# Kernel tuning notes

Measured on AMD Instinct MI355X. Metric: run time of the kernel, lower is better.

The kernel has to match this reference:

```python
import jax, jax.numpy as jnp
import numpy as np

H = 64
IN_DIM = 32
N = 50000
E = 100000
B = 500


def setup_inputs() -> dict:
    key = jax.random.key(0)
    ks = jax.random.split(key, 16)
    def rn(k, shape, s=0.05):
        return jax.random.normal(k, shape, dtype=jnp.float32) * s
    inp = dict(
        nfeat=rn(ks[0], (N, IN_DIM), 1.0),
        efeat=rn(ks[1], (E, 5), 1.0),
        lin0_w=rn(ks[2], (IN_DIM, H)), lin0_b=jnp.zeros((H,), jnp.float32),
        ew1=rn(ks[3], (5, 128)), eb1=jnp.zeros((128,), jnp.float32),
        ew2=rn(ks[4], (128, H * H)), eb2=jnp.zeros((H * H,), jnp.float32),
        conv_b=jnp.zeros((H,), jnp.float32),
        gru_wih=rn(ks[5], (3 * H, H)), gru_whh=rn(ks[6], (3 * H, H)),
        gru_bih=jnp.zeros((3 * H,), jnp.float32), gru_bhh=jnp.zeros((3 * H,), jnp.float32),
        lstm_wih=rn(ks[7], (4 * H, 2 * H)), lstm_whh=rn(ks[8], (4 * H, H)),
        lstm_bih=jnp.zeros((4 * H,), jnp.float32), lstm_bhh=jnp.zeros((4 * H,), jnp.float32),
        fc1_w=rn(ks[9], (2 * H, H)), fc1_b=jnp.zeros((H,), jnp.float32),
        fc2_w=rn(ks[10], (H, 1)), fc2_b=jnp.zeros((1,), jnp.float32),
        src=jax.random.randint(ks[11], (E,), 0, N),
        dst=jax.random.randint(ks[12], (E,), 0, N),
        graph_id=jnp.arange(N) // (N // B),  # B graphs of equal size, sorted
        num_graphs=B,
    )
    return inp


def reference(nfeat, efeat, lin0_w, lin0_b, ew1, eb1, ew2, eb2, conv_b,
              gru_wih, gru_whh, gru_bih, gru_bhh,
              lstm_wih, lstm_whh, lstm_bih, lstm_bhh,
              fc1_w, fc1_b, fc2_w, fc2_b,
              src, dst, graph_id, num_graphs):
    n_nodes = nfeat.shape[0]
    # lin0 + relu
    h = jax.nn.relu(nfeat @ lin0_w + lin0_b)  # [N, H]
    # edge-conditioned weight matrices (same for all 3 iterations)
    We = (jax.nn.relu(efeat @ ew1 + eb1) @ ew2 + eb2).reshape(-1, H, H)  # [E, H, H]
    deg = jnp.maximum(
        jax.ops.segment_sum(jnp.ones(src.shape[0], jnp.float32), dst, num_segments=n_nodes), 1.0)
    for _ in range(3):
        # NNConv: gather src feats, per-edge matmul, scatter-mean at dst
        msg = jnp.einsum('eh,eho->eo', h[src], We)  # [E, H]
        agg = jax.ops.segment_sum(msg, dst, num_segments=n_nodes) / deg[:, None]
        m = jax.nn.relu(agg + conv_b)
        # GRU step (PyTorch gate order r,z,n)
        gi = m @ gru_wih.T + gru_bih
        gh = h @ gru_whh.T + gru_bhh
        r = jax.nn.sigmoid(gi[:, :H] + gh[:, :H])
        z = jax.nn.sigmoid(gi[:, H:2 * H] + gh[:, H:2 * H])
        n = jnp.tanh(gi[:, 2 * H:] + r * gh[:, 2 * H:])
        h = (1.0 - z) * n + z * h
    feat = h  # [N, H]
    # Set2Set pooling: 3 iters, 1-layer LSTM with input 2H
    q_star = jnp.zeros((num_graphs, 2 * H), jnp.float32)
    hh = jnp.zeros((num_graphs, H), jnp.float32)
    cc = jnp.zeros((num_graphs, H), jnp.float32)
    for _ in range(3):
        gates = q_star @ lstm_wih.T + lstm_bih + hh @ lstm_whh.T + lstm_bhh
        i = jax.nn.sigmoid(gates[:, :H])
        f = jax.nn.sigmoid(gates[:, H:2 * H])
        g = jnp.tanh(gates[:, 2 * H:3 * H])
        o = jax.nn.sigmoid(gates[:, 3 * H:])
        cc = f * cc + i * g
        hh = o * jnp.tanh(cc)
        q = hh  # [B, H]
        e = jnp.sum(feat * q[graph_id], axis=-1)  # [N]
        emax = jax.ops.segment_max(e, graph_id, num_segments=num_graphs)
        alpha = jnp.exp(e - emax[graph_id])
        denom = jax.ops.segment_sum(alpha, graph_id, num_segments=num_graphs)
        alpha = alpha / denom[graph_id]
        readout = jax.ops.segment_sum(alpha[:, None] * feat, graph_id, num_segments=num_graphs)
        q_star = jnp.concatenate([q, readout], axis=-1)  # [B, 2H]
    pred = jax.nn.relu(q_star @ fc1_w + fc1_b) @ fc2_w + fc2_b  # [B, 1]
    return pred.reshape(-1)
```

## Files before the change

kernel.cpp:

```cpp
#include <hip/hip_runtime.h>

#define HD 64
#define NNODE 50000
#define NEDGE 100000
#define NGR 500
#define NPG 100
#define EPAD 100352
#define NCH 66
#define NUPL 65

typedef _Float16 f16;
typedef _Float16 f16x2 __attribute__((ext_vector_type(2)));
typedef _Float16 f16x8 __attribute__((ext_vector_type(8)));
typedef float f32x4 __attribute__((ext_vector_type(4)));

__device__ __forceinline__ float sigmoidf_(float x) { return 1.f / (1.f + __expf(-x)); }

__device__ __forceinline__ void gload16(const void* g, void* l) {
    __builtin_amdgcn_global_load_lds((const __attribute__((address_space(1))) unsigned int*)g,
                                     (__attribute__((address_space(3))) unsigned int*)l, 16, 0, 0);
}

#define G_NODE 12500
#define G_EMLP 392
#define G_GRU  48
#define G_T1   128
#define G_T2   64
#define G_IDX  392
#define G_ALL (G_NODE + G_EMLP + G_GRU + G_T1 + G_T2 + G_IDX)

__global__ __launch_bounds__(256) void k_prep_all(
    const float* __restrict__ nfeat, const float* __restrict__ lin0_w, const float* __restrict__ lin0_b,
    const float* __restrict__ efeat, const float* __restrict__ ew1, const float* __restrict__ eb1,
    const float* __restrict__ gwih, const float* __restrict__ gwhh,
    const float* __restrict__ lwih, const float* __restrict__ lwhh,
    const int* __restrict__ src, const int* __restrict__ dst,
    float* __restrict__ h, f16x2* __restrict__ uP,
    f16* __restrict__ gB1, f16* __restrict__ gB2,
    float* __restrict__ lwihT, float* __restrict__ lwhhT,
    int* __restrict__ srcP, int* __restrict__ dstP, int* __restrict__ cnt) {
    int bb = blockIdx.x;
    int t = threadIdx.x;
    if (bb < G_NODE) {
        int idx = bb * 256 + t;
        int n = idx >> 6, o = idx & 63;
        if (n >= NNODE) return;
        const float* nf = nfeat + n * 32;
        float acc = lin0_b[o];
#pragma unroll
        for (int i = 0; i < 32; i++) acc += nf[i] * lin0_w[i * 64 + o];
        h[idx] = fmaxf(acc, 0.f);
        return;
    }
    bb -= G_NODE;
    if (bb < G_EMLP) {
        __shared__ float sw[5 * 128];
        __shared__ float sb[128];
        for (int idx = t; idx < 640; idx += 256) sw[idx] = ew1[idx];
        if (t < 128) sb[t] = eb1[t];
        __syncthreads();
        int e = bb * 256 + t;
        bool valid = e < NEDGE;
        float ef[5];
#pragma unroll
        for (int i = 0; i < 5; i++) ef[i] = valid ? efeat[e * 5 + i] : 0.f;
#pragma unroll 2
        for (int c = 0; c < 64; c++) {
            float v[2];
#pragma unroll
            for (int s = 0; s < 2; s++) {
                int k = 2 * c + s;
                float acc = sb[k];
#pragma unroll
                for (int i = 0; i < 5; i++) acc += ef[i] * sw[i * 128 + k];
                v[s] = valid ? fmaxf(acc, 0.f) : 0.f;
            }
            f16x2 pv;
            pv[0] = (f16)v[0];
            pv[1] = (f16)v[1];
            uP[(size_t)c * EPAD + e] = pv;
        }
        {
            f16x2 pv;
            pv[0] = valid ? (f16)1.f : (f16)0.f;
            pv[1] = pv[0];
            uP[(size_t)64 * EPAD + e] = pv;
        }
        return;
    }
    bb -= G_EMLP;
    if (bb < G_GRU) {
        int idx = bb * 256 + t;
        int cp = idx >> 6, k = idx & 63;
        int w = cp / 48, rem = cp % 48;
        int tg = rem >> 4, cc = rem & 15;
        int orow = tg * 64 + w * 16 + cc;
        gB1[idx] = (f16)gwih[orow * 64 + k];
        gB2[idx] = (f16)gwhh[orow * 64 + k];
        return;
    }
    bb -= G_GRU;
    if (bb < G_T1) {
        int idx = bb * 256 + t;
        int r = idx >> 7, c = idx & 127;
        lwihT[c * 256 + r] = lwih[idx];
        return;
    }
    bb -= G_T1;
    if (bb < G_T2) {
        int idx = bb * 256 + t;
        int r = idx >> 6, c = idx & 63;
        lwhhT[c * 256 + r] = lwhh[idx];
        return;
    }
    bb -= G_T2;
    {
        int e = bb * 256 + t;
        if (e >= EPAD) return;
        if (e < NEDGE) {
            int d = dst[e];
            srcP[e] = src[e];
            dstP[e] = d;
            atomicAdd(&cnt[d], 1);
        } else {
            srcP[e] = 0;
            dstP[e] = -1;
        }
    }
}

__global__ __launch_bounds__(256) void k_pack_b(const float* __restrict__ ew2,
                                                const float* __restrict__ eb2,
                                                f16* __restrict__ w2hp) {
    __shared__ float s[8192];
    int c = blockIdx.x, t = threadIdx.x;
    for (int i = t; i < 8192; i += 256) {
        int kg = c * 128 + (i >> 6);
        float v = 0.f;
        if (kg < 8192) v = ew2[(size_t)c * 8192 + i];
        else if (kg < 8256) v = eb2[(kg - 8192) * 64 + (i & 63)];
        s[i] = v;
    }
    __syncthreads();
    f16* outp = w2hp + (size_t)c * 8192 + t * 32;
#pragma unroll
    for (int ff = 0; ff < 4; ff++) {
        int F = t * 4 + ff;
        int l = F & 63;
        int jj = (F >> 6) & 3;
        int sl = (F >> 8) & 3;
        f16x8 v;
#pragma unroll
        for (int q = 0; q < 8; q++)
            v[q] = (f16)s[(sl * 32 + ((l >> 4) << 3) + q) * 64 + jj * 16 + (l & 15)];
        *(f16x8*)(outp + ff * 8) = v;
    }
}

__global__ __launch_bounds__(128) void k_msg(
    const float* __restrict__ h, const f16x2* __restrict__ uP, const f16* __restrict__ w2hp,
    const int* __restrict__ srcP, const int* __restrict__ dstP, float* __restrict__ agg) {
    __shared__ __attribute__((aligned(16))) f16 sB[2 * 8192];
    int t = threadIdx.x;
    int w = t >> 6, l = t & 63;
    int eb = blockIdx.x * 128 + w * 64;
    int lr = l & 15, lg = l >> 4;
    f16x8 xf[4][2];
#pragma unroll
    for (int i = 0; i < 4; i++) {
        const float* xb = h + (size_t)srcP[eb + i * 16 + lr] * 64;
#pragma unroll
        for (int p = 0; p < 2; p++) {
            float4 v0 = *(const float4*)(xb + p * 32 + lg * 8);
            float4 v1 = *(const float4*)(xb + p * 32 + lg * 8 + 4);
            f16x8 xv;
            xv[0] = (f16)v0.x; xv[1] = (f16)v0.y; xv[2] = (f16)v0.z; xv[3] = (f16)v0.w;
            xv[4] = (f16)v1.x; xv[5] = (f16)v1.y; xv[6] = (f16)v1.z; xv[7] = (f16)v1.w;
            xf[i][p] = xv;
        }
    }
    const f16x8* gB = (const f16x8*)w2hp;
    f16x8* sB8 = (f16x8*)sB;
#pragma unroll
    for (int i = 0; i < 8; i++)
        gload16(gB + i * 128 + t, sB8 + i * 128 + t);
    f32x4 acc[4][4];
#pragma unroll
    for (int i = 0; i < 4; i++)
#pragma unroll
        for (int j = 0; j < 4; j++) acc[i][j] = (f32x4){0.f, 0.f, 0.f, 0.f};
    f16x2 uc[4], un[4];
#pragma unroll
    for (int i = 0; i < 4; i++) uc[i] = uP[eb + i * 16 + lr];
    __syncthreads();
#pragma unroll 1
    for (int c = 0; c <= 64; c++) {
        int buf = c & 1;
        if (c < 64) {
            const f16x8* gs = gB + (size_t)(c + 1) * 1024;
            f16x8* ld = sB8 + (buf ^ 1) * 1024;
#pragma unroll
            for (int i = 0; i < 8; i++)
                gload16(gs + i * 128 + t, ld + i * 128 + t);
            int cn = c + 1;
#pragma unroll
            for (int i = 0; i < 4; i++) un[i] = uP[(size_t)cn * EPAD + eb + i * 16 + lr];
        }
        f16x8 bf[4][4];
#pragma unroll
        for (int s = 0; s < 4; s++)
#pragma unroll
            for (int j = 0; j < 4; j++)
                bf[s][j] = sB8[buf * 1024 + s * 256 + j * 64 + l];
        __builtin_amdgcn_s_setprio(1);
#pragma unroll
        for (int s = 0; s < 4; s++) {
#pragma unroll
            for (int i = 0; i < 4; i++) {
                f16x8 av = xf[i][s & 1] * uc[i][s >> 1];
#pragma unroll
                for (int j = 0; j < 4; j++)
                    acc[i][j] = __builtin_amdgcn_mfma_f32_16x16x32_f16(av, bf[s][j], acc[i][j], 0, 0, 0);
            }
        }
        __builtin_amdgcn_s_setprio(0);
#pragma unroll
        for (int i = 0; i < 4; i++) uc[i] = un[i];
        __syncthreads();
    }
#pragma unroll
    for (int i = 0; i < 4; i++) {
        int rb = eb + i * 16 + lg * 4;
        int4 d4 = *(const int4*)(dstP + rb);
#pragma unroll
        for (int r = 0; r < 4; r++) {
            int d = (r == 0) ? d4.x : (r == 1) ? d4.y : (r == 2) ? d4.z : d4.w;
            if (d >= 0) {
                float* ap = agg + (size_t)d * 64 + lr;
#pragma unroll
                for (int j = 0; j < 4; j++) atomicAdd(ap + j * 16, acc[i][j][r]);
            }
        }
    }
}

#define GWP 72
__global__ __launch_bounds__(256) void k_gru2(float* __restrict__ agg,
                                              const int* __restrict__ cnt,
                                              const float* __restrict__ convb,
                                              const f16* __restrict__ B1g,
                                              const f16* __restrict__ B2g,
                                              const float* __restrict__ bih,
                                              const float* __restrict__ bhh,
                                              float* __restrict__ h) {
    __shared__ f16 sM[64 * GWP];
    __shared__ f16 sH[64 * GWP];
    int t = threadIdx.x;
    int nb = blockIdx.x * 64;
    int w = t >> 6, l = t & 63, lr = l & 15, lg = l >> 4;
    f16x8 b1[2][3], b2[2][3];
#pragma unroll
    for (int kk = 0; kk < 2; kk++)
#pragma unroll
        for (int j = 0; j < 3; j++) {
            size_t off = (size_t)(w * 48 + j * 16 + lr) * 64 + kk * 32 + lg * 8;
            b1[kk][j] = *(const f16x8*)(B1g + off);
            b2[kk][j] = *(const f16x8*)(B2g + off);
        }
#pragma unroll
    for (int it = 0; it < 16; it++) {
        int idx = t + 256 * it;
        int node = idx >> 6, k = idx & 63;
        int gn = nb + node;
        float mv = 0.f, hv = 0.f;
        if (gn < NNODE) {
            size_t off = (size_t)gn * 64 + k;
            float dinv = 1.f / (float)max(cnt[gn], 1);
            mv = fmaxf(agg[off] * dinv + convb[k], 0.f);
            hv = h[off];
            agg[off] = 0.f;
        }
        sM[node * GWP + k] = (f16)mv;
        sH[node * GWP + k] = (f16)hv;
    }
    __syncthreads();
    f32x4 aih[4][3], ahh[4][3];
#pragma unroll
    for (int i = 0; i < 4; i++)
#pragma unroll
        for (int j = 0; j < 3; j++) {
            aih[i][j] = (f32x4){0.f, 0.f, 0.f, 0.f};
            ahh[i][j] = (f32x4){0.f, 0.f, 0.f, 0.f};
        }
#pragma unroll
    for (int kk = 0; kk < 2; kk++) {
        f16x8 am[4], ah[4];
#pragma unroll
        for (int i = 0; i < 4; i++) {
            am[i] = *(const f16x8*)(sM + (i * 16 + lr) * GWP + kk * 32 + lg * 8);
            ah[i] = *(const f16x8*)(sH + (i * 16 + lr) * GWP + kk * 32 + lg * 8);
        }
#pragma unroll
        for (int i = 0; i < 4; i++)
#pragma unroll
            for (int j = 0; j < 3; j++) {
                aih[i][j] = __builtin_amdgcn_mfma_f32_16x16x32_f16(am[i], b1[kk][j], aih[i][j], 0, 0, 0);
                ahh[i][j] = __builtin_amdgcn_mfma_f32_16x16x32_f16(ah[i], b2[kk][j], ahh[i][j], 0, 0, 0);
            }
    }
    float bi0 = bih[0 * 64 + w * 16 + lr], bh0 = bhh[0 * 64 + w * 16 + lr];
    float bi1 = bih[1 * 64 + w * 16 + lr], bh1 = bhh[1 * 64 + w * 16 + lr];
    float bi2 = bih[2 * 64 + w * 16 + lr], bh2 = bhh[2 * 64 + w * 16 + lr];
#pragma unroll
    for (int i = 0; i < 4; i++)
#pragma unroll
        for (int r = 0; r < 4; r++) {
            int node = i * 16 + lg * 4 + r;
            int gn = nb + node;
            if (gn >= NNODE) continue;
            float rg = sigmoidf_(aih[i][0][r] + bi0 + ahh[i][0][r] + bh0);
            float z = sigmoidf_(aih[i][1][r] + bi1 + ahh[i][1][r] + bh1);
            float nn = tanhf(aih[i][2][r] + bi2 + rg * (ahh[i][2][r] + bh2));
            size_t off = (size_t)gn * 64 + w * 16 + lr;
            float hold = h[off];
            h[off] = (1.f - z) * nn + z * hold;
        }
}

#define FP 68
__global__ __launch_bounds__(256) void k_s2s(const float* __restrict__ feat,
                                             const float* __restrict__ wihT,
                                             const float* __restrict__ whhT,
                                             const float* __restrict__ lbih,
                                             const float* __restrict__ lbhh,
                                             const float* __restrict__ fc1w,
                                             const float* __restrict__ fc1b,
                                             const float* __restrict__ fc2w,
                                             const float* __restrict__ fc2b,
                                             float* __restrict__ out) {
    __shared__ float sf[NPG * FP];
    __shared__ float sq[128];
    __shared__ float sh[64], scc[64];
    __shared__ float sg[256];
    __shared__ float se[NPG];
    __shared__ float red[2];
    int g = blockIdx.x, t = threadIdx.x;
    const float* fb = feat + (size_t)g * NPG * 64;
    for (int idx = t; idx < NPG * 64; idx += 256)
        sf[(idx >> 6) * FP + (idx & 63)] = fb[idx];
    if (t < 128) sq[t] = 0.f;
    if (t >= 128 && t < 192) { sh[t - 128] = 0.f; scc[t - 128] = 0.f; }
    __syncthreads();
    for (int it = 0; it < 3; it++) {
        float gate = lbih[t] + lbhh[t];
#pragma unroll 8
        for (int i = 0; i < 128; i++) gate += sq[i] * wihT[i * 256 + t];
#pragma unroll 8
        for (int i = 0; i < 64; i++) gate += sh[i] * whhT[i * 256 + t];
        sg[t] = gate;
        __syncthreads();
        if (t < 64) {
            float ig = sigmoidf_(sg[t]);
            float fg = sigmoidf_(sg[64 + t]);
            float gg = tanhf(sg[128 + t]);
            float og = sigmoidf_(sg[192 + t]);
            float c = fg * scc[t] + ig * gg;
            scc[t] = c;
            float hv = og * tanhf(c);
            sh[t] = hv;
            sq[t] = hv;
        }
        __syncthreads();
        if (t < NPG) {
            float e = 0.f;
#pragma unroll 8
            for (int o = 0; o < 64; o++) e += sf[t * FP + o] * sh[o];
            se[t] = e;
        }
        __syncthreads();
        if (t < 64) {
            float m = -1e30f;
            for (int i2 = t; i2 < NPG; i2 += 64) m = fmaxf(m, se[i2]);
            for (int d = 32; d; d >>= 1) m = fmaxf(m, __shfl_down(m, d));
            if (t == 0) red[0] = m;
        }
        __syncthreads();
        float emax = red[0];
        if (t < NPG) se[t] = __expf(se[t] - emax);
        __syncthreads();
        if (t < 64) {
            float s = 0.f;
            for (int i2 = t; i2 < NPG; i2 += 64) s += se[i2];
            for (int d = 32; d; d >>= 1) s += __shfl_down(s, d);
            if (t == 0) red[1] = s;
        }
        __syncthreads();
        if (t < 64) {
            float dnv = 1.f / red[1];
            float r = 0.f;
#pragma unroll 4
            for (int n = 0; n < NPG; n++) r += se[n] * sf[n * FP + t];
            sq[64 + t] = r * dnv;
        }
        __syncthreads();
    }
    if (t < 64) {
        float hsum = fc1b[t];
#pragma unroll 8
        for (int i = 0; i < 128; i++) hsum += sq[i] * fc1w[i * 64 + t];
        float p = fmaxf(hsum, 0.f) * fc2w[t];
        for (int d = 32; d; d >>= 1) p += __shfl_down(p, d);
        if (t == 0) out[g] = p + fc2b[0];
    }
}

extern "C" void kernel_launch(void* const* d_in, const int* in_sizes, int n_in,
                              void* d_out, int out_size, void* d_ws, size_t ws_size,
                              hipStream_t stream) {
    const float* nfeat = (const float*)d_in[0];
    const float* efeat = (const float*)d_in[1];
    const float* lin0_w = (const float*)d_in[2];
    const float* lin0_b = (const float*)d_in[3];
    const float* ew1 = (const float*)d_in[4];
    const float* eb1 = (const float*)d_in[5];
    const float* ew2 = (const float*)d_in[6];
    const float* eb2 = (const float*)d_in[7];
    const float* convb = (const float*)d_in[8];
    const float* gwih = (const float*)d_in[9];
    const float* gwhh = (const float*)d_in[10];
    const float* gbih = (const float*)d_in[11];
    const float* gbhh = (const float*)d_in[12];
    const float* lwih = (const float*)d_in[13];
    const float* lwhh = (const float*)d_in[14];
    const float* lbih = (const float*)d_in[15];
    const float* lbhh = (const float*)d_in[16];
    const float* fc1w = (const float*)d_in[17];
    const float* fc1b = (const float*)d_in[18];
    const float* fc2w = (const float*)d_in[19];
    const float* fc2b = (const float*)d_in[20];
    const int* src = (const int*)d_in[21];
    const int* dst = (const int*)d_in[22];
    float* out = (float*)d_out;

    char* p = (char*)d_ws;
    auto alloc = [&](size_t bytes) {
        char* q = p;
        p += (bytes + 255) & ~(size_t)255;
        return q;
    };
    f16x2* uP = (f16x2*)alloc((size_t)NUPL * EPAD * 4);
    f16* w2hp = (f16*)alloc((size_t)NCH * 8192 * 2);
    float* h = (float*)alloc((size_t)NNODE * 64 * 4);
    float* agg = (float*)alloc((size_t)NNODE * 64 * 4);
    int* cnt = (int*)alloc((size_t)NNODE * 4);
    float* lwihT = (float*)alloc((size_t)128 * 256 * 4);
    float* lwhhT = (float*)alloc((size_t)64 * 256 * 4);
    f16* gB1 = (f16*)alloc((size_t)12288 * 2);
    f16* gB2 = (f16*)alloc((size_t)12288 * 2);
    int* srcP = (int*)alloc((size_t)EPAD * 4);
    int* dstP = (int*)alloc((size_t)EPAD * 4);
    if ((size_t)(p - (char*)d_ws) > ws_size) return;

    hipMemsetAsync(cnt, 0, (size_t)NNODE * 4, stream);
    hipMemsetAsync(agg, 0, (size_t)NNODE * 64 * 4, stream);

    k_prep_all<<<G_ALL, 256, 0, stream>>>(nfeat, lin0_w, lin0_b, efeat, ew1, eb1,
                                          gwih, gwhh, lwih, lwhh, src, dst,
                                          h, uP, gB1, gB2, lwihT, lwhhT, srcP, dstP, cnt);
    k_pack_b<<<NCH, 256, 0, stream>>>(ew2, eb2, w2hp);

    for (int it = 0; it < 3; it++) {
        k_msg<<<EPAD / 128, 128, 0, stream>>>(h, uP, w2hp, srcP, dstP, agg);
        k_gru2<<<(NNODE + 63) / 64, 256, 0, stream>>>(agg, cnt, convb, gB1, gB2, gbih, gbhh, h);
    }
    k_s2s<<<NGR, 256, 0, stream>>>(h, lwihT, lwhhT, lbih, lbhh, fc1w, fc1b, fc2w, fc2b, out);
}
```

Before: 486.1 us.

## Triple-buffer edge-weight chunks in k_msg with explicit vmcnt waits

Switches the per-chunk shared-memory staging of the edge-MLP weight slices from double to triple buffering. The prefetch is issued two chunks ahead, and explicit s_waitcnt vmcnt counts with raw barriers replace __syncthreads. The aim is to hide global-to-LDS load latency behind MFMA work instead of stalling each iteration. In exchange it uses 1.5x the LDS per block, which may reduce occupancy, and the hand-counted vmcnt values must match the number of outstanding loads to stay correct.

After: 694.0 us. 42.8% more time.

```diff
diff --git a/kernel.cpp b/kernel.cpp
--- a/kernel.cpp
+++ b/kernel.cpp
@@ -157,10 +157,43 @@
     }
 }
 
+#define CHUNK_STEP(CC, WAITSTR, STG)                                                        \
+    {                                                                                       \
+        int bufc = (CC) % 3;                                                                \
+        asm volatile(WAITSTR ::: "memory");                                                 \
+        __builtin_amdgcn_s_barrier();                                                       \
+        f16x8 bf[4][4];                                                                     \
+        _Pragma("unroll") for (int s = 0; s < 4; s++)                                       \
+            _Pragma("unroll") for (int j = 0; j < 4; j++)                                   \
+                bf[s][j] = sB8[bufc * 1024 + s * 256 + j * 64 + l];                         \
+        f16x2 un[4];                                                                        \
+        if ((CC) < 64) {                                                                    \
+            _Pragma("unroll") for (int i = 0; i < 4; i++)                                   \
+                un[i] = uP[(size_t)((CC) + 1) * EPAD + eb + i * 16 + lr];                   \
+        }                                                                                   \
+        __builtin_amdgcn_s_setprio(1);                                                      \
+        _Pragma("unroll") for (int s = 0; s < 4; s++)                                       \
+            _Pragma("unroll") for (int i = 0; i < 4; i++) {                                 \
+                f16x8 av = xf[i][s & 1] * uc[i][s >> 1];                                    \
+                _Pragma("unroll") for (int j = 0; j < 4; j++)                               \
+                    acc[i][j] = __builtin_amdgcn_mfma_f32_16x16x32_f16(av, bf[s][j],        \
+                                                                      acc[i][j], 0, 0, 0); \
+            }                                                                               \
+        __builtin_amdgcn_s_setprio(0);                                                      \
+        __builtin_amdgcn_s_barrier();                                                       \
+        if (STG) {                                                                          \
+            const f16x8* gs = gB + (size_t)((CC) + 3) * 1024;                               \
+            f16x8* ld = sB8 + bufc * 1024;                                                  \
+            _Pragma("unroll") for (int i = 0; i < 8; i++)                                   \
+                gload16(gs + i * 128 + t, ld + i * 128 + t);                                \
+        }                                                                                   \
+        _Pragma("unroll") for (int i = 0; i < 4; i++) uc[i] = un[i];                        \
+    }
+
 __global__ __launch_bounds__(128) void k_msg(
     const float* __restrict__ h, const f16x2* __restrict__ uP, const f16* __restrict__ w2hp,
     const int* __restrict__ srcP, const int* __restrict__ dstP, float* __restrict__ agg) {
-    __shared__ __attribute__((aligned(16))) f16 sB[2 * 8192];
+    __shared__ __attribute__((aligned(16))) f16 sB[3 * 8192];
     int t = threadIdx.x;
     int w = t >> 6, l = t & 63;
     int eb = blockIdx.x * 128 + w * 64;
@@ -181,53 +214,26 @@
     }
     const f16x8* gB = (const f16x8*)w2hp;
     f16x8* sB8 = (f16x8*)sB;
-#pragma unroll
-    for (int i = 0; i < 8; i++)
-        gload16(gB + i * 128 + t, sB8 + i * 128 + t);
+    f16x2 uc[4];
+#pragma unroll
+    for (int i = 0; i < 4; i++) uc[i] = uP[eb + i * 16 + lr];
+#pragma unroll
+    for (int cc = 0; cc < 3; cc++)
+#pragma unroll
+        for (int i = 0; i < 8; i++)
+            gload16(gB + (size_t)cc * 1024 + i * 128 + t, sB8 + cc * 1024 + i * 128 + t);
     f32x4 acc[4][4];
 #pragma unroll
     for (int i = 0; i < 4; i++)
 #pragma unroll
         for (int j = 0; j < 4; j++) acc[i][j] = (f32x4){0.f, 0.f, 0.f, 0.f};
-    f16x2 uc[4], un[4];
-#pragma unroll
-    for (int i = 0; i < 4; i++) uc[i] = uP[eb + i * 16 + lr];
-    __syncthreads();
 #pragma unroll 1
-    for (int c = 0; c <= 64; c++) {
-        int buf = c & 1;
-        if (c < 64) {
-            const f16x8* gs = gB + (size_t)(c + 1) * 1024;
-            f16x8* ld = sB8 + (buf ^ 1) * 1024;
-#pragma unroll
-            for (int i = 0; i < 8; i++)
-                gload16(gs + i * 128 + t, ld + i * 128 + t);
-            int cn = c + 1;
-#pragma unroll
-            for (int i = 0; i < 4; i++) un[i] = uP[(size_t)cn * EPAD + eb + i * 16 + lr];
-        }
-        f16x8 bf[4][4];
-#pragma unroll
-        for (int s = 0; s < 4; s++)
-#pragma unroll
-            for (int j = 0; j < 4; j++)
-                bf[s][j] = sB8[buf * 1024 + s * 256 + j * 64 + l];
-        __builtin_amdgcn_s_setprio(1);
-#pragma unroll
-        for (int s = 0; s < 4; s++) {
-#pragma unroll
-            for (int i = 0; i < 4; i++) {
-                f16x8 av = xf[i][s & 1] * uc[i][s >> 1];
-#pragma unroll
-                for (int j = 0; j < 4; j++)
-                    acc[i][j] = __builtin_amdgcn_mfma_f32_16x16x32_f16(av, bf[s][j], acc[i][j], 0, 0, 0);
-            }
-        }
-        __builtin_amdgcn_s_setprio(0);
-#pragma unroll
-        for (int i = 0; i < 4; i++) uc[i] = un[i];
-        __syncthreads();
-    }
+    for (int c = 0; c < 62; c++) {
+        CHUNK_STEP(c, "s_waitcnt vmcnt(12)", (c <= 61))
+    }
+    CHUNK_STEP(62, "s_waitcnt vmcnt(12)", false)
+    CHUNK_STEP(63, "s_waitcnt vmcnt(4)", false)
+    CHUNK_STEP(64, "s_waitcnt vmcnt(0)", false)
 #pragma unroll
     for (int i = 0; i < 4; i++) {
         int rb = eb + i * 16 + lg * 4;
```
